# Kernel optimization log

Hardware: AMD Instinct MI355X
Metric: run time of the kernel (lower is better)

## Reference

```python
import jax, jax.numpy as jnp
import numpy as np

# Model dims (match init_kwargs)
M = 4          # bits per symbol
T = 32         # spike-encoding timesteps
F = 41         # input_features (tap window)
H = 256        # hidden_features
O = 16         # output_features
B = 4096       # batch

# LIF parameters (norse LIFParameters as constructed in __init__)
DT = 0.001
ALPHA = 100.0
V_TH = 1.0
V_LEAK = 0.0
V_RESET = 0.0
TAU_MEM_INV = 100.0
TAU_SYN_INV = 200.0


@jax.custom_vjp
def spike(x):
    # norse heaviside with SuperSpike surrogate gradient
    return (x > 0).astype(x.dtype)

def _spike_fwd(x):
    return spike(x), x

def _spike_bwd(x, g):
    return (g / (ALPHA * jnp.abs(x) + 1.0) ** 2,)

spike.defvjp(_spike_fwd, _spike_bwd)


def setup_inputs() -> dict:
    key = jax.random.key(0)
    ks = jax.random.split(key, 6)
    x = jax.random.randint(ks[0], (B, F), 0, 2 ** M)  # symbol indices
    # nn.Embedding default init: N(0,1)
    emb = jax.random.normal(ks[1], (2 ** M, M * T), dtype=jnp.float32)
    # nn.Linear default init: U(-1/sqrt(fan_in), 1/sqrt(fan_in))
    s_in = 1.0 / np.sqrt(M * F)
    W_in = jax.random.uniform(ks[2], (H, M * F), minval=-s_in, maxval=s_in, dtype=jnp.float32)
    W_rec = jax.random.normal(ks[3], (H, H), dtype=jnp.float32) / np.sqrt(H)
    W_rec = W_rec * (1.0 - jnp.eye(H, dtype=jnp.float32))  # autapses=False: zero diagonal
    s_out = 1.0 / np.sqrt(H)
    W_out = jax.random.uniform(ks[4], (O, H), minval=-s_out, maxval=s_out, dtype=jnp.float32)
    b_out = jax.random.uniform(ks[5], (O,), minval=-s_out, maxval=s_out, dtype=jnp.float32)
    return {"x": x, "emb": emb, "W_in": W_in, "W_rec": W_rec, "W_out": W_out, "b_out": b_out}


def reference(x, emb, W_in, W_rec, W_out, b_out):
    b = x.shape[0]
    xe = emb[x]                                      # (B, F, M*T)
    xe = xe.reshape(b, T, M * F).transpose(1, 0, 2)  # (T, B, M*F)

    z0 = jnp.zeros((b, H), jnp.float32)
    v0 = jnp.full((b, H), V_LEAK, jnp.float32)
    i0 = jnp.zeros((b, H), jnp.float32)

    def step(carry, xt):
        z, v, i = carry
        # LIF dynamics (norse lif_step): decay membrane & synaptic current
        v_dec = v + DT * TAU_MEM_INV * ((V_LEAK - v) + i)
        i_dec = i * (1.0 - DT * TAU_SYN_INV)
        z_new = spike(v_dec - V_TH)
        v_new = (1.0 - z_new) * v_dec + z_new * V_RESET
        # new current: feedforward input + recurrence on PREVIOUS spikes
        i_new = i_dec + xt @ W_in.T + z @ W_rec.T
        out_t = z_new @ W_out.T + b_out
        return (z_new, v_new, i_new), (z_new, out_t)

    _, (spikes, outs) = jax.lax.scan(step, (z0, v0, i0), xe)
    spikerate = jnp.sum(spikes) / (T * b * H)
    z_sum = jnp.sum(outs, axis=0)  # decode: sum over timesteps -> (B, O)
    return z_sum, spikerate
```

## Files before the change

### kernel.cpp

```cpp
#include <hip/hip_runtime.h>


typedef float f32x4 __attribute__((ext_vector_type(4)));

#define T_STEPS 32
#define FDIM    41
#define ODIM    16
#define BDIM    4096
#define MF      164

#define P_FLOATS  (32 * 3 * 16 * 256)
#define WT_ROWS   257
#define WT_FLOATS (WT_ROWS * 256)

#define HAS3(T) ((((T) * MF) & 127) > 92)

__global__ __launch_bounds__(256) void k_prep(const float* __restrict__ emb,
                                              const float* __restrict__ W_in,
                                              const float* __restrict__ W_rec,
                                              float* __restrict__ P,
                                              float* __restrict__ WT,
                                              int* __restrict__ counter)
{
    const int bid = blockIdx.x;
    const int tid = threadIdx.x;

    if (bid < 384) {
        const int g  = bid & 3;
        const int ts = bid >> 2;
        const int t  = ts / 3;
        const int si = ts % 3;
        const int k0   = t * MF;
        const int f    = (k0 >> 7) + si;
        const int base = f << 7;
        const int c0   = max(k0, base) - base;
        const int c1   = min(k0 + MF, base + 128) - base;
        const int len  = c1 - c0;

        if (len <= 0) {
            #pragma unroll
            for (int s = 0; s < 4; ++s)
                P[((t * 3 + si) * 16 + 4 * g + s) * 256 + tid] = 0.0f;
            return;
        }

        __shared__ float emb_lds[4][128];
        for (int idx = tid; idx < 4 * 128; idx += 256) {
            const int s = idx >> 7, u = idx & 127;
            if (u < len) emb_lds[s][u] = emb[((4 * g + s) << 7) + c0 + u];
        }
        __syncthreads();

        const int j0 = base + c0 - k0;
        double a0 = 0.0, a1 = 0.0, a2 = 0.0, a3 = 0.0;
        for (int u = 0; u < len; ++u) {
            const double w = (double)W_in[tid * MF + j0 + u];
            a0 += w * (double)emb_lds[0][u];
            a1 += w * (double)emb_lds[1][u];
            a2 += w * (double)emb_lds[2][u];
            a3 += w * (double)emb_lds[3][u];
        }
        P[((t * 3 + si) * 16 + 4 * g + 0) * 256 + tid] = (float)a0;
        P[((t * 3 + si) * 16 + 4 * g + 1) * 256 + tid] = (float)a1;
        P[((t * 3 + si) * 16 + 4 * g + 2) * 256 + tid] = (float)a2;
        P[((t * 3 + si) * 16 + 4 * g + 3) * 256 + tid] = (float)a3;
    } else {
        const int h = bid - 384;
        if (h < 256) {
            WT[h * 256 + tid] = W_rec[tid * 256 + h];
        } else {
            WT[256 * 256 + tid] = 0.0f;
            if (tid == 0) *counter = 0;
        }
    }
}

__global__ __launch_bounds__(256) void k_main(const int* __restrict__ x,
                                              const float* __restrict__ P,
                                              const float* __restrict__ WT,
                                              const float* __restrict__ W_out,
                                              const float* __restrict__ b_out,
                                              float* __restrict__ out,
                                              int* __restrict__ counter)
{
#pragma clang fp contract(off)
    __shared__ float cnt_lds[4][256];
    __shared__ int   red[4];

    const int tid  = threadIdx.x;
    const int lane = tid & 63;
    const int wv   = __builtin_amdgcn_readfirstlane(tid >> 6);
    const int b    = blockIdx.x * 4 + wv;

    const f32x4* __restrict__ P4  = (const f32x4*)P;
    const f32x4* __restrict__ WT4 = (const f32x4*)WT;

    const int xv = (lane < FDIM) ? x[b * FDIM + lane] : 0;
    int sym[FDIM];
    #pragma unroll
    for (int f = 0; f < FDIM; ++f)
        sym[f] = __builtin_amdgcn_readlane(xv, f);

    const f32x4 zero4 = {0.f, 0.f, 0.f, 0.f};
    f32x4 vm = zero4, cur = zero4;
    int n0 = 0, n1 = 0, n2 = 0, n3 = 0;

    f32x4 pA0 = zero4, pA1 = zero4, pA2 = zero4;
    f32x4 pB0 = zero4, pB1 = zero4, pB2 = zero4;
    f32x4 wA0 = zero4, wA1 = zero4, wA2 = zero4, wA3 = zero4;
    f32x4 wB0 = zero4, wB1 = zero4, wB2 = zero4, wB3 = zero4;
    f32x4 rextA = zero4, rextB = zero4;
    int cntA = 0, cntB = 0;

    pA0 = P4[(0 * 16 + sym[0]) * 64 + lane];
    pA1 = P4[(1 * 16 + sym[1]) * 64 + lane];

    #define PEEL(dst)                                                         \
        do {                                                                  \
            if (m0)      { dst = 4 * __builtin_ctzll(m0) + 0; m0 &= m0 - 1; } \
            else if (m1) { dst = 4 * __builtin_ctzll(m1) + 1; m1 &= m1 - 1; } \
            else if (m2) { dst = 4 * __builtin_ctzll(m2) + 2; m2 &= m2 - 1; } \
            else if (m3) { dst = 4 * __builtin_ctzll(m3) + 3; m3 &= m3 - 1; } \
        } while (0)

    #define STEP(TC, C, N, LAST)                                              \
    {                                                                         \
                                      \
        const f32x4 vdec = vm + 0.1f * (cur - vm);                            \
        const f32x4 idec = cur * 0.8f;                                        \
        const bool z0 = vdec.x > 1.0f, z1 = vdec.y > 1.0f,                    \
                   z2 = vdec.z > 1.0f, z3 = vdec.w > 1.0f;                    \
        unsigned long long m0 = __ballot(z0), m1 = __ballot(z1),              \
                           m2 = __ballot(z2), m3 = __ballot(z3);              \
        vm.x = z0 ? 0.0f : vdec.x;  vm.y = z1 ? 0.0f : vdec.y;                \
        vm.z = z2 ? 0.0f : vdec.z;  vm.w = z3 ? 0.0f : vdec.w;                \
        n0 += z0; n1 += z1; n2 += z2; n3 += z3;                               \
                                          \
        f32x4 ff = p##C##0 + p##C##1;                                         \
        if (HAS3(TC)) ff = ff + p##C##2;                                      \
        f32x4 rec = rext##C;                                                  \
        if (cnt##C > 0) { rec += w##C##0; rec += w##C##1;                     \
                          rec += w##C##2; rec += w##C##3; }                   \
        cur = (idec + ff) + rec;                                              \
                          \
        if (!(LAST)) {                                                        \
            const int f0_ = (((TC) + 1) * MF) >> 7;                           \
            p##N##0 = P4[((((TC) + 1) * 3 + 0) * 16 + sym[f0_    ]) * 64 + lane]; \
            p##N##1 = P4[((((TC) + 1) * 3 + 1) * 16 + sym[f0_ + 1]) * 64 + lane]; \
            if (HAS3((TC) + 1))                                               \
                p##N##2 = P4[((((TC) + 1) * 3 + 2) * 16 + sym[f0_ + 2]) * 64 + lane]; \
        }                                                                     \
                                \
        if (!(LAST)) {                                                        \
            const int c = __popcll(m0) + __popcll(m1)                         \
                        + __popcll(m2) + __popcll(m3);                        \
            cnt##N = c;                                                       \
            rext##N = zero4;                                                  \
            if (c > 0) {                                                      \
                int u0 = 256, u1 = 256, u2 = 256, u3 = 256;                   \
                PEEL(u0); PEEL(u1); PEEL(u2); PEEL(u3);                       \
                w##N##0 = WT4[u0 * 64 + lane];                                \
                w##N##1 = WT4[u1 * 64 + lane];                                \
                w##N##2 = WT4[u2 * 64 + lane];                                \
                w##N##3 = WT4[u3 * 64 + lane];                                \
                if (c > 4) {                     \
                    while (m0) { const int l = __builtin_ctzll(m0); m0 &= m0 - 1; \
                                 rext##N += WT4[(4 * l + 0) * 64 + lane]; }   \
                    while (m1) { const int l = __builtin_ctzll(m1); m1 &= m1 - 1; \
                                 rext##N += WT4[(4 * l + 1) * 64 + lane]; }   \
                    while (m2) { const int l = __builtin_ctzll(m2); m2 &= m2 - 1; \
                                 rext##N += WT4[(4 * l + 2) * 64 + lane]; }   \
                    while (m3) { const int l = __builtin_ctzll(m3); m3 &= m3 - 1; \
                                 rext##N += WT4[(4 * l + 3) * 64 + lane]; }   \
                }                                                             \
            }                                                                 \
        }                                                                     \
    }

    STEP( 0, A, B, 0)  STEP( 1, B, A, 0)  STEP( 2, A, B, 0)  STEP( 3, B, A, 0)
    STEP( 4, A, B, 0)  STEP( 5, B, A, 0)  STEP( 6, A, B, 0)  STEP( 7, B, A, 0)
    STEP( 8, A, B, 0)  STEP( 9, B, A, 0)  STEP(10, A, B, 0)  STEP(11, B, A, 0)
    STEP(12, A, B, 0)  STEP(13, B, A, 0)  STEP(14, A, B, 0)  STEP(15, B, A, 0)
    STEP(16, A, B, 0)  STEP(17, B, A, 0)  STEP(18, A, B, 0)  STEP(19, B, A, 0)
    STEP(20, A, B, 0)  STEP(21, B, A, 0)  STEP(22, A, B, 0)  STEP(23, B, A, 0)
    STEP(24, A, B, 0)  STEP(25, B, A, 0)  STEP(26, A, B, 0)  STEP(27, B, A, 0)
    STEP(28, A, B, 0)  STEP(29, B, A, 0)  STEP(30, A, B, 0)  STEP(31, B, A, 1)

    #undef STEP
    #undef PEEL

    cnt_lds[wv][4 * lane + 0] = (float)n0;
    cnt_lds[wv][4 * lane + 1] = (float)n1;
    cnt_lds[wv][4 * lane + 2] = (float)n2;
    cnt_lds[wv][4 * lane + 3] = (float)n3;

    int myspk = n0 + n1 + n2 + n3;
    #pragma unroll
    for (int off = 32; off > 0; off >>= 1)
        myspk += __shfl_down(myspk, off, 64);
    if (lane == 0) red[wv] = myspk;

    __syncthreads();
    if (tid == 0) atomicAdd(counter, red[0] + red[1] + red[2] + red[3]);

    {
        const int o = lane & 15;
        const int q = lane >> 4;
        const float* __restrict__ wo = W_out + o * 256 + q * 64;
        const float* __restrict__ cl = cnt_lds[wv] + q * 64;
        float acc = 0.0f;
        #pragma unroll 8
        for (int h = 0; h < 64; ++h)
            acc += cl[h] * wo[h];
        acc += __shfl_down(acc, 16, 64);
        acc += __shfl_down(acc, 32, 64);
        if (q == 0)
            out[b * ODIM + o] = 32.0f * b_out[o] + acc;
    }
}

__global__ void k_fin(const int* __restrict__ counter, float* __restrict__ out)
{
    out[BDIM * ODIM] = (float)(*counter) * (1.0f / 33554432.0f);
}

extern "C" void kernel_launch(void* const* d_in, const int* in_sizes, int n_in,
                              void* d_out, int out_size, void* d_ws, size_t ws_size,
                              hipStream_t stream)
{
    const int*   x     = (const int*)  d_in[0];
    const float* emb   = (const float*)d_in[1];
    const float* W_in  = (const float*)d_in[2];
    const float* W_rec = (const float*)d_in[3];
    const float* W_out = (const float*)d_in[4];
    const float* b_out = (const float*)d_in[5];
    float* out = (float*)d_out;

    float* P       = (float*)d_ws;
    float* WT      = P + P_FLOATS;
    int*   counter = (int*)(WT + WT_FLOATS);

    k_prep<<<384 + 257, 256, 0, stream>>>(emb, W_in, W_rec, P, WT, counter);
    k_main<<<BDIM / 4, 256, 0, stream>>>(x, P, WT, W_out, b_out, out, counter);
    k_fin<<<1, 1, 0, stream>>>(counter, out);
}
```

Measured before the change: 47.73 us.

## Precombine symbol-pair input projections and deepen prefetch pipeline

Adds a k_comb kernel that builds a table of summed projections for every pair of adjacent symbols per timestep. The main loop can then fetch one pre-summed vector instead of two, and only does so when the workspace is large enough. The feedforward prefetch now runs two steps ahead with triple buffering, the recurrent weight gathers are issued only for as many spikes as exist, and a sched_barrier is placed per step. The cost is an extra launch, a 2MB table, and a different floating-point summation order.

Measured after the change: 52.46 us. 1.1x slower.

```diff
diff --git a/kernel.cpp b/kernel.cpp
--- a/kernel.cpp
+++ b/kernel.cpp
@@ -9,9 +9,14 @@
 #define BDIM    4096
 #define MF      164
 
-#define P_FLOATS  (32 * 3 * 16 * 256)
-#define WT_ROWS   257
-#define WT_FLOATS (WT_ROWS * 256)
+#define P_FLOATS   (32 * 3 * 16 * 256)
+#define WT_ROWS    257
+#define WT_FLOATS  (WT_ROWS * 256)
+#define P2_FLOATS  (32 * 16 * 16 * 256)
+#define WT_OFF     (P_FLOATS * 4)
+#define CNT_OFF    ((P_FLOATS + WT_FLOATS) * 4)
+#define P2_OFF     (CNT_OFF + 16)
+#define WS_NEED    (P2_OFF + P2_FLOATS * 4)
 
 #define HAS3(T) ((((T) * MF) & 127) > 92)
 
@@ -75,8 +80,24 @@
     }
 }
 
+__global__ __launch_bounds__(256) void k_comb(const float* __restrict__ P,
+                                              float* __restrict__ P2)
+{
+    const int t  = blockIdx.x >> 4;
+    const int s0 = blockIdx.x & 15;
+    const int h  = threadIdx.x;
+    const float a = P[((t * 3 + 0) * 16 + s0) * 256 + h];
+    const float* __restrict__ pb = P + ((t * 3 + 1) * 16) * 256 + h;
+    float* __restrict__ dst = P2 + ((t * 16 + s0) * 16) * 256 + h;
+    #pragma unroll
+    for (int s1 = 0; s1 < 16; ++s1)
+        dst[s1 * 256] = a + pb[s1 * 256];
+}
+
+template <bool USEP2>
 __global__ __launch_bounds__(256) void k_main(const int* __restrict__ x,
                                               const float* __restrict__ P,
+                                              const float* __restrict__ P2,
                                               const float* __restrict__ WT,
                                               const float* __restrict__ W_out,
                                               const float* __restrict__ b_out,
@@ -92,8 +113,9 @@
     const int wv   = __builtin_amdgcn_readfirstlane(tid >> 6);
     const int b    = blockIdx.x * 4 + wv;
 
-    const f32x4* __restrict__ P4  = (const f32x4*)P;
-    const f32x4* __restrict__ WT4 = (const f32x4*)WT;
+    const f32x4* __restrict__ P4   = (const f32x4*)P;
+    const f32x4* __restrict__ P2_4 = (const f32x4*)P2;
+    const f32x4* __restrict__ WT4  = (const f32x4*)WT;
 
     const int xv = (lane < FDIM) ? x[b * FDIM + lane] : 0;
     int sym[FDIM];
@@ -105,15 +127,23 @@
     f32x4 vm = zero4, cur = zero4;
     int n0 = 0, n1 = 0, n2 = 0, n3 = 0;
 
-    f32x4 pA0 = zero4, pA1 = zero4, pA2 = zero4;
-    f32x4 pB0 = zero4, pB1 = zero4, pB2 = zero4;
+    f32x4 p0a = zero4, p0b = zero4, p1a = zero4, p1b = zero4,
+          p2a = zero4, p2b = zero4;
+    f32x4 qA = zero4, qB = zero4;
     f32x4 wA0 = zero4, wA1 = zero4, wA2 = zero4, wA3 = zero4;
     f32x4 wB0 = zero4, wB1 = zero4, wB2 = zero4, wB3 = zero4;
     f32x4 rextA = zero4, rextB = zero4;
     int cntA = 0, cntB = 0;
 
-    pA0 = P4[(0 * 16 + sym[0]) * 64 + lane];
-    pA1 = P4[(1 * 16 + sym[1]) * 64 + lane];
+    if constexpr (USEP2) {
+        p0a = P2_4[((0 * 16 + sym[0]) * 16 + sym[1]) * 64 + lane];
+        p1a = P2_4[((1 * 16 + sym[1]) * 16 + sym[2]) * 64 + lane];
+    } else {
+        p0a = P4[(0 * 16 + sym[0]) * 64 + lane];
+        p0b = P4[(1 * 16 + sym[1]) * 64 + lane];
+        p1a = P4[((3 + 0) * 16 + sym[1]) * 64 + lane];
+        p1b = P4[((3 + 1) * 16 + sym[2]) * 64 + lane];
+    }
 
     #define PEEL(dst)                                                         \
         do {                                                                  \
@@ -123,7 +153,7 @@
             else if (m3) { dst = 4 * __builtin_ctzll(m3) + 3; m3 &= m3 - 1; } \
         } while (0)
 
-    #define STEP(TC, C, N, LAST)                                              \
+    #define STEP(TC, PC, PN, WC, WN, LAST)                                    \
     {                                                                         \
                                       \
         const f32x4 vdec = vm + 0.1f * (cur - vm);                            \
@@ -136,55 +166,75 @@
         vm.z = z2 ? 0.0f : vdec.z;  vm.w = z3 ? 0.0f : vdec.w;                \
         n0 += z0; n1 += z1; n2 += z2; n3 += z3;                               \
                                           \
-        f32x4 ff = p##C##0 + p##C##1;                                         \
-        if (HAS3(TC)) ff = ff + p##C##2;                                      \
-        f32x4 rec = rext##C;                                                  \
-        if (cnt##C > 0) { rec += w##C##0; rec += w##C##1;                     \
-                          rec += w##C##2; rec += w##C##3; }                   \
+        f32x4 ff;                                                             \
+        if constexpr (USEP2) ff = PC##a; else ff = PC##a + PC##b;             \
+        if (HAS3(TC)) ff = ff + q##WC;                                        \
+        f32x4 rec = rext##WC;                                                 \
+        if (cnt##WC > 0) rec += w##WC##0;                                     \
+        if (cnt##WC > 1) rec += w##WC##1;                                     \
+        if (cnt##WC > 2) rec += w##WC##2;                                     \
+        if (cnt##WC > 3) rec += w##WC##3;                                     \
         cur = (idec + ff) + rec;                                              \
-                          \
+                       \
+        if ((TC) + 2 < T_STEPS) {                                             \
+            const int f0_ = (((TC) + 2) * MF) >> 7;                           \
+            if constexpr (USEP2) {                                            \
+                PN##a = P2_4[((((TC) + 2) * 16 + sym[f0_]) * 16               \
+                              + sym[f0_ + 1]) * 64 + lane];                   \
+            } else {                                                          \
+                PN##a = P4[((((TC) + 2) * 3 + 0) * 16 + sym[f0_    ]) * 64 + lane]; \
+                PN##b = P4[((((TC) + 2) * 3 + 1) * 16 + sym[f0_ + 1]) * 64 + lane]; \
+            }                                                                 \
+        }                                                                     \
+                                      \
+        if ((TC) + 1 < T_STEPS && HAS3((TC) + 1)) {                           \
+            const int f0q = (((TC) + 1) * MF) >> 7;                           \
+            q##WN = P4[((((TC) + 1) * 3 + 2) * 16 + sym[f0q + 2]) * 64 + lane]; \
+        }                                                                     \
+                              \
         if (!(LAST)) {                                                        \
-            const int f0_ = (((TC) + 1) * MF) >> 7;                           \
-            p##N##0 = P4[((((TC) + 1) * 3 + 0) * 16 + sym[f0_    ]) * 64 + lane]; \
-            p##N##1 = P4[((((TC) + 1) * 3 + 1) * 16 + sym[f0_ + 1]) * 64 + lane]; \
-            if (HAS3((TC) + 1))                                               \
-                p##N##2 = P4[((((TC) + 1) * 3 + 2) * 16 + sym[f0_ + 2]) * 64 + lane]; \
-        }                                                                     \
-                                \
-        if (!(LAST)) {                                                        \
-            const int c = __popcll(m0) + __popcll(m1)                         \
-                        + __popcll(m2) + __popcll(m3);                        \
-            cnt##N = c;                                                       \
-            rext##N = zero4;                                                  \
-            if (c > 0) {                                                      \
-                int u0 = 256, u1 = 256, u2 = 256, u3 = 256;                   \
-                PEEL(u0); PEEL(u1); PEEL(u2); PEEL(u3);                       \
-                w##N##0 = WT4[u0 * 64 + lane];                                \
-                w##N##1 = WT4[u1 * 64 + lane];                                \
-                w##N##2 = WT4[u2 * 64 + lane];                                \
-                w##N##3 = WT4[u3 * 64 + lane];                                \
-                if (c > 4) {                     \
-                    while (m0) { const int l = __builtin_ctzll(m0); m0 &= m0 - 1; \
-                                 rext##N += WT4[(4 * l + 0) * 64 + lane]; }   \
-                    while (m1) { const int l = __builtin_ctzll(m1); m1 &= m1 - 1; \
-                                 rext##N += WT4[(4 * l + 1) * 64 + lane]; }   \
-                    while (m2) { const int l = __builtin_ctzll(m2); m2 &= m2 - 1; \
-                                 rext##N += WT4[(4 * l + 2) * 64 + lane]; }   \
-                    while (m3) { const int l = __builtin_ctzll(m3); m3 &= m3 - 1; \
-                                 rext##N += WT4[(4 * l + 3) * 64 + lane]; }   \
+            const int c_ = __popcll(m0) + __popcll(m1)                        \
+                         + __popcll(m2) + __popcll(m3);                       \
+            cnt##WN = c_;                                                     \
+            rext##WN = zero4;                                                 \
+            if (c_ > 0) {                                                     \
+                int u_ = 256;                                                 \
+                PEEL(u_); w##WN##0 = WT4[u_ * 64 + lane];                     \
+                if (c_ > 1) {                                                 \
+                    PEEL(u_); w##WN##1 = WT4[u_ * 64 + lane];                 \
+                    if (c_ > 2) {                                             \
+                        PEEL(u_); w##WN##2 = WT4[u_ * 64 + lane];             \
+                        if (c_ > 3) {                                         \
+                            PEEL(u_); w##WN##3 = WT4[u_ * 64 + lane];         \
+                            if (c_ > 4) {        \
+                                while (m0) { const int l = __builtin_ctzll(m0); m0 &= m0 - 1; \
+                                             rext##WN += WT4[(4 * l + 0) * 64 + lane]; } \
+                                while (m1) { const int l = __builtin_ctzll(m1); m1 &= m1 - 1; \
+                                             rext##WN += WT4[(4 * l + 1) * 64 + lane]; } \
+                                while (m2) { const int l = __builtin_ctzll(m2); m2 &= m2 - 1; \
+                                             rext##WN += WT4[(4 * l + 2) * 64 + lane]; } \
+                                while (m3) { const int l = __builtin_ctzll(m3); m3 &= m3 - 1; \
+                                             rext##WN += WT4[(4 * l + 3) * 64 + lane]; } \
+                            }                                                 \
+                        }                                                     \
+                    }                                                         \
                 }                                                             \
             }                                                                 \
         }                                                                     \
-    }
-
-    STEP( 0, A, B, 0)  STEP( 1, B, A, 0)  STEP( 2, A, B, 0)  STEP( 3, B, A, 0)
-    STEP( 4, A, B, 0)  STEP( 5, B, A, 0)  STEP( 6, A, B, 0)  STEP( 7, B, A, 0)
-    STEP( 8, A, B, 0)  STEP( 9, B, A, 0)  STEP(10, A, B, 0)  STEP(11, B, A, 0)
-    STEP(12, A, B, 0)  STEP(13, B, A, 0)  STEP(14, A, B, 0)  STEP(15, B, A, 0)
-    STEP(16, A, B, 0)  STEP(17, B, A, 0)  STEP(18, A, B, 0)  STEP(19, B, A, 0)
-    STEP(20, A, B, 0)  STEP(21, B, A, 0)  STEP(22, A, B, 0)  STEP(23, B, A, 0)
-    STEP(24, A, B, 0)  STEP(25, B, A, 0)  STEP(26, A, B, 0)  STEP(27, B, A, 0)
-    STEP(28, A, B, 0)  STEP(29, B, A, 0)  STEP(30, A, B, 0)  STEP(31, B, A, 1)
+        __builtin_amdgcn_sched_barrier(0);                                    \
+    }
+
+    STEP( 0, p0, p2, A, B, 0)  STEP( 1, p1, p0, B, A, 0)  STEP( 2, p2, p1, A, B, 0)
+    STEP( 3, p0, p2, B, A, 0)  STEP( 4, p1, p0, A, B, 0)  STEP( 5, p2, p1, B, A, 0)
+    STEP( 6, p0, p2, A, B, 0)  STEP( 7, p1, p0, B, A, 0)  STEP( 8, p2, p1, A, B, 0)
+    STEP( 9, p0, p2, B, A, 0)  STEP(10, p1, p0, A, B, 0)  STEP(11, p2, p1, B, A, 0)
+    STEP(12, p0, p2, A, B, 0)  STEP(13, p1, p0, B, A, 0)  STEP(14, p2, p1, A, B, 0)
+    STEP(15, p0, p2, B, A, 0)  STEP(16, p1, p0, A, B, 0)  STEP(17, p2, p1, B, A, 0)
+    STEP(18, p0, p2, A, B, 0)  STEP(19, p1, p0, B, A, 0)  STEP(20, p2, p1, A, B, 0)
+    STEP(21, p0, p2, B, A, 0)  STEP(22, p1, p0, A, B, 0)  STEP(23, p2, p1, B, A, 0)
+    STEP(24, p0, p2, A, B, 0)  STEP(25, p1, p0, B, A, 0)  STEP(26, p2, p1, A, B, 0)
+    STEP(27, p0, p2, B, A, 0)  STEP(28, p1, p0, A, B, 0)  STEP(29, p2, p1, B, A, 0)
+    STEP(30, p0, p2, A, B, 0)  STEP(31, p1, p0, B, A, 1)
 
     #undef STEP
     #undef PEEL
@@ -236,11 +286,22 @@
     const float* b_out = (const float*)d_in[5];
     float* out = (float*)d_out;
 
-    float* P       = (float*)d_ws;
-    float* WT      = P + P_FLOATS;
-    int*   counter = (int*)(WT + WT_FLOATS);
+    char* ws = (char*)d_ws;
+    float* P       = (float*)ws;
+    float* WT      = (float*)(ws + WT_OFF);
+    int*   counter = (int*)  (ws + CNT_OFF);
+    float* P2      = (float*)(ws + P2_OFF);
+
+    const bool useP2 = (ws_size >= (size_t)WS_NEED);
 
     k_prep<<<384 + 257, 256, 0, stream>>>(emb, W_in, W_rec, P, WT, counter);
-    k_main<<<BDIM / 4, 256, 0, stream>>>(x, P, WT, W_out, b_out, out, counter);
+    if (useP2) {
+        k_comb<<<32 * 16, 256, 0, stream>>>(P, P2);
+        k_main<true><<<BDIM / 4, 256, 0, stream>>>(x, P, P2, WT, W_out, b_out,
+                                                   out, counter);
+    } else {
+        k_main<false><<<BDIM / 4, 256, 0, stream>>>(x, P, P2, WT, W_out, b_out,
+                                                    out, counter);
+    }
     k_fin<<<1, 1, 0, stream>>>(counter, out);
 }
```

## Prefetch up to eight recurrent rows via inline asm loads with explicit waitcnt

Applied to the files above, without the earlier changes.

Rewrites the per-timestep loop so the first eight spiking neurons' W_rec rows are issued as asynchronous inline-asm global loads for the next step. The step then waits with an explicit vmcnt(0) and a scheduling barrier before consuming them. Symbol indices are read per-use with readlane instead of being held in a 41-entry array, and launch bounds request 4 blocks per CU to cut register use and raise occupancy. The goal is to overlap more gather latency with the serial LIF update. The cost is that the full waitcnt serialises every outstanding load, including the in-loop rext gathers, and hand-written asm limits the compiler's scheduling.

New measurement: 67.04 us. 1.4x slower.

```diff
diff --git a/kernel.cpp b/kernel.cpp
--- a/kernel.cpp
+++ b/kernel.cpp
@@ -9,11 +9,17 @@
 #define BDIM    4096
 #define MF      164
 
-#define P_FLOATS  (32 * 3 * 16 * 256)
-#define WT_ROWS   257
-#define WT_FLOATS (WT_ROWS * 256)
+#define P_FLOATS   (32 * 3 * 16 * 256)
+#define WT_ROWS    257
+#define WT_FLOATS  (WT_ROWS * 256)
 
 #define HAS3(T) ((((T) * MF) & 127) > 92)
+
+__device__ __forceinline__ f32x4 gload(const f32x4* p) {
+    f32x4 r;
+    asm volatile("global_load_dwordx4 %0, %1, off" : "=&v"(r) : "v"(p));
+    return r;
+}
 
 __global__ __launch_bounds__(256) void k_prep(const float* __restrict__ emb,
                                               const float* __restrict__ W_in,
@@ -75,13 +81,13 @@
     }
 }
 
-__global__ __launch_bounds__(256) void k_main(const int* __restrict__ x,
-                                              const float* __restrict__ P,
-                                              const float* __restrict__ WT,
-                                              const float* __restrict__ W_out,
-                                              const float* __restrict__ b_out,
-                                              float* __restrict__ out,
-                                              int* __restrict__ counter)
+__global__ __launch_bounds__(256, 4) void k_main(const int* __restrict__ x,
+                                                 const float* __restrict__ P,
+                                                 const float* __restrict__ WT,
+                                                 const float* __restrict__ W_out,
+                                                 const float* __restrict__ b_out,
+                                                 float* __restrict__ out,
+                                                 int* __restrict__ counter)
 {
 #pragma clang fp contract(off)
     __shared__ float cnt_lds[4][256];
@@ -96,97 +102,86 @@
     const f32x4* __restrict__ WT4 = (const f32x4*)WT;
 
     const int xv = (lane < FDIM) ? x[b * FDIM + lane] : 0;
-    int sym[FDIM];
+
+    const f32x4 zero4 = {0.f, 0.f, 0.f, 0.f};
+    f32x4 vm = zero4;
+    f32x4 cur = zero4;
+    f32x4 rext = zero4;
+    f32x4 s0 = zero4, s1 = zero4, s2 = zero4, s3 = zero4,
+          s4 = zero4, s5 = zero4, s6 = zero4, s7 = zero4;
+    f32x4 pf0 = zero4, pf1 = zero4, pf2 = zero4;
+    int cg = 0;
+    int n0 = 0, n1 = 0, n2 = 0, n3 = 0;
+
+    pf0 = gload(P4 + (0 * 16 + __builtin_amdgcn_readlane(xv, 0)) * 64 + lane);
+    pf1 = gload(P4 + (1 * 16 + __builtin_amdgcn_readlane(xv, 1)) * 64 + lane);
+
+    #define PEEL(dst)                                                          \
+        if (h0)      { dst = 4*(int)__builtin_ctzll(h0)+0; h0 &= h0-1; }       \
+        else if (h1) { dst = 4*(int)__builtin_ctzll(h1)+1; h1 &= h1-1; }       \
+        else if (h2) { dst = 4*(int)__builtin_ctzll(h2)+2; h2 &= h2-1; }       \
+        else if (h3) { dst = 4*(int)__builtin_ctzll(h3)+3; h3 &= h3-1; }
+
     #pragma unroll
-    for (int f = 0; f < FDIM; ++f)
-        sym[f] = __builtin_amdgcn_readlane(xv, f);
-
-    const f32x4 zero4 = {0.f, 0.f, 0.f, 0.f};
-    f32x4 vm = zero4, cur = zero4;
-    int n0 = 0, n1 = 0, n2 = 0, n3 = 0;
-
-    f32x4 pA0 = zero4, pA1 = zero4, pA2 = zero4;
-    f32x4 pB0 = zero4, pB1 = zero4, pB2 = zero4;
-    f32x4 wA0 = zero4, wA1 = zero4, wA2 = zero4, wA3 = zero4;
-    f32x4 wB0 = zero4, wB1 = zero4, wB2 = zero4, wB3 = zero4;
-    f32x4 rextA = zero4, rextB = zero4;
-    int cntA = 0, cntB = 0;
-
-    pA0 = P4[(0 * 16 + sym[0]) * 64 + lane];
-    pA1 = P4[(1 * 16 + sym[1]) * 64 + lane];
-
-    #define PEEL(dst)                                                         \
-        do {                                                                  \
-            if (m0)      { dst = 4 * __builtin_ctzll(m0) + 0; m0 &= m0 - 1; } \
-            else if (m1) { dst = 4 * __builtin_ctzll(m1) + 1; m1 &= m1 - 1; } \
-            else if (m2) { dst = 4 * __builtin_ctzll(m2) + 2; m2 &= m2 - 1; } \
-            else if (m3) { dst = 4 * __builtin_ctzll(m3) + 3; m3 &= m3 - 1; } \
-        } while (0)
-
-    #define STEP(TC, C, N, LAST)                                              \
-    {                                                                         \
-                                      \
-        const f32x4 vdec = vm + 0.1f * (cur - vm);                            \
-        const f32x4 idec = cur * 0.8f;                                        \
-        const bool z0 = vdec.x > 1.0f, z1 = vdec.y > 1.0f,                    \
-                   z2 = vdec.z > 1.0f, z3 = vdec.w > 1.0f;                    \
-        unsigned long long m0 = __ballot(z0), m1 = __ballot(z1),              \
-                           m2 = __ballot(z2), m3 = __ballot(z3);              \
-        vm.x = z0 ? 0.0f : vdec.x;  vm.y = z1 ? 0.0f : vdec.y;                \
-        vm.z = z2 ? 0.0f : vdec.z;  vm.w = z3 ? 0.0f : vdec.w;                \
-        n0 += z0; n1 += z1; n2 += z2; n3 += z3;                               \
-                                          \
-        f32x4 ff = p##C##0 + p##C##1;                                         \
-        if (HAS3(TC)) ff = ff + p##C##2;                                      \
-        f32x4 rec = rext##C;                                                  \
-        if (cnt##C > 0) { rec += w##C##0; rec += w##C##1;                     \
-                          rec += w##C##2; rec += w##C##3; }                   \
-        cur = (idec + ff) + rec;                                              \
-                          \
-        if (!(LAST)) {                                                        \
-            const int f0_ = (((TC) + 1) * MF) >> 7;                           \
-            p##N##0 = P4[((((TC) + 1) * 3 + 0) * 16 + sym[f0_    ]) * 64 + lane]; \
-            p##N##1 = P4[((((TC) + 1) * 3 + 1) * 16 + sym[f0_ + 1]) * 64 + lane]; \
-            if (HAS3((TC) + 1))                                               \
-                p##N##2 = P4[((((TC) + 1) * 3 + 2) * 16 + sym[f0_ + 2]) * 64 + lane]; \
-        }                                                                     \
-                                \
-        if (!(LAST)) {                                                        \
-            const int c = __popcll(m0) + __popcll(m1)                         \
-                        + __popcll(m2) + __popcll(m3);                        \
-            cnt##N = c;                                                       \
-            rext##N = zero4;                                                  \
-            if (c > 0) {                                                      \
-                int u0 = 256, u1 = 256, u2 = 256, u3 = 256;                   \
-                PEEL(u0); PEEL(u1); PEEL(u2); PEEL(u3);                       \
-                w##N##0 = WT4[u0 * 64 + lane];                                \
-                w##N##1 = WT4[u1 * 64 + lane];                                \
-                w##N##2 = WT4[u2 * 64 + lane];                                \
-                w##N##3 = WT4[u3 * 64 + lane];                                \
-                if (c > 4) {                     \
-                    while (m0) { const int l = __builtin_ctzll(m0); m0 &= m0 - 1; \
-                                 rext##N += WT4[(4 * l + 0) * 64 + lane]; }   \
-                    while (m1) { const int l = __builtin_ctzll(m1); m1 &= m1 - 1; \
-                                 rext##N += WT4[(4 * l + 1) * 64 + lane]; }   \
-                    while (m2) { const int l = __builtin_ctzll(m2); m2 &= m2 - 1; \
-                                 rext##N += WT4[(4 * l + 2) * 64 + lane]; }   \
-                    while (m3) { const int l = __builtin_ctzll(m3); m3 &= m3 - 1; \
-                                 rext##N += WT4[(4 * l + 3) * 64 + lane]; }   \
-                }                                                             \
-            }                                                                 \
-        }                                                                     \
+    for (int t = 0; t < T_STEPS; ++t) {
+        const f32x4 vdec = vm + 0.1f * (cur - vm);
+        const bool z0 = vdec.x > 1.0f, z1 = vdec.y > 1.0f,
+                   z2 = vdec.z > 1.0f, z3 = vdec.w > 1.0f;
+        const unsigned long long m0 = __ballot(z0), m1 = __ballot(z1),
+                                 m2 = __ballot(z2), m3 = __ballot(z3);
+        vm.x = z0 ? 0.0f : vdec.x;  vm.y = z1 ? 0.0f : vdec.y;
+        vm.z = z2 ? 0.0f : vdec.z;  vm.w = z3 ? 0.0f : vdec.w;
+        n0 += z0; n1 += z1; n2 += z2; n3 += z3;
+
+        unsigned long long h0 = m0, h1 = m1, h2 = m2, h3 = m3;
+        const int cg_ = __popcll(h0) + __popcll(h1)
+                      + __popcll(h2) + __popcll(h3);
+        int ua = 256, ub = 256, uc = 256, ud = 256,
+            ue = 256, uf = 256, ug = 256, uh = 256;
+        PEEL(ua) PEEL(ub) PEEL(uc) PEEL(ud)
+        PEEL(ue) PEEL(uf) PEEL(ug) PEEL(uh)
+
+        asm volatile("s_waitcnt vmcnt(0)" ::: "memory");
+        __builtin_amdgcn_sched_barrier(0);
+
+        f32x4 rec = rext;
+        if (cg > 0) { rec += s0; rec += s1; }
+        if (cg > 2) { rec += s2; rec += s3; }
+        if (cg > 4) { rec += s4; rec += s5; }
+        if (cg > 6) { rec += s6; rec += s7; }
+        f32x4 ff = pf0 + pf1;
+        if (HAS3(t)) ff += pf2;
+        cur = (cur * 0.8f + ff) + rec;
+
+        if (t + 1 < T_STEPS) {
+            rext = zero4;
+            while (h0) { const int r = 4*(int)__builtin_ctzll(h0)+0; h0 &= h0-1;
+                         rext += WT4[r * 64 + lane]; }
+            while (h1) { const int r = 4*(int)__builtin_ctzll(h1)+1; h1 &= h1-1;
+                         rext += WT4[r * 64 + lane]; }
+            while (h2) { const int r = 4*(int)__builtin_ctzll(h2)+2; h2 &= h2-1;
+                         rext += WT4[r * 64 + lane]; }
+            while (h3) { const int r = 4*(int)__builtin_ctzll(h3)+3; h3 &= h3-1;
+                         rext += WT4[r * 64 + lane]; }
+
+            if (cg_ > 0) { s0 = gload(WT4 + ua * 64 + lane);
+                           s1 = gload(WT4 + ub * 64 + lane); }
+            if (cg_ > 2) { s2 = gload(WT4 + uc * 64 + lane);
+                           s3 = gload(WT4 + ud * 64 + lane); }
+            if (cg_ > 4) { s4 = gload(WT4 + ue * 64 + lane);
+                           s5 = gload(WT4 + uf * 64 + lane); }
+            if (cg_ > 6) { s6 = gload(WT4 + ug * 64 + lane);
+                           s7 = gload(WT4 + uh * 64 + lane); }
+            cg = cg_;
+
+            const int tn = t + 1;
+            const int f0 = (tn * MF) >> 7;
+            pf0 = gload(P4 + ((tn*3 + 0)*16 + __builtin_amdgcn_readlane(xv, f0    )) * 64 + lane);
+            pf1 = gload(P4 + ((tn*3 + 1)*16 + __builtin_amdgcn_readlane(xv, f0 + 1)) * 64 + lane);
+            if (HAS3(tn))
+                pf2 = gload(P4 + ((tn*3 + 2)*16 + __builtin_amdgcn_readlane(xv, f0 + 2)) * 64 + lane);
+        }
     }
-
-    STEP( 0, A, B, 0)  STEP( 1, B, A, 0)  STEP( 2, A, B, 0)  STEP( 3, B, A, 0)
-    STEP( 4, A, B, 0)  STEP( 5, B, A, 0)  STEP( 6, A, B, 0)  STEP( 7, B, A, 0)
-    STEP( 8, A, B, 0)  STEP( 9, B, A, 0)  STEP(10, A, B, 0)  STEP(11, B, A, 0)
-    STEP(12, A, B, 0)  STEP(13, B, A, 0)  STEP(14, A, B, 0)  STEP(15, B, A, 0)
-    STEP(16, A, B, 0)  STEP(17, B, A, 0)  STEP(18, A, B, 0)  STEP(19, B, A, 0)
-    STEP(20, A, B, 0)  STEP(21, B, A, 0)  STEP(22, A, B, 0)  STEP(23, B, A, 0)
-    STEP(24, A, B, 0)  STEP(25, B, A, 0)  STEP(26, A, B, 0)  STEP(27, B, A, 0)
-    STEP(28, A, B, 0)  STEP(29, B, A, 0)  STEP(30, A, B, 0)  STEP(31, B, A, 1)
-
-    #undef STEP
     #undef PEEL
 
     cnt_lds[wv][4 * lane + 0] = (float)n0;
```
